# Kernel tuning notes

Hardware: AMD Instinct MI355X
Metric: run time of the kernel (lower is better)

The kernel has to match this reference:

```python
import jax, jax.numpy as jnp
import numpy as np

K_ORDER = 3
GRID_N = 10
GRID_LO, GRID_HI = -2.0, 2.0
LAYERS = [(49, 256), (256, 256), (256, 10)]
NCOEF = GRID_N + K_ORDER  # 13


def mish(x):
    return x * jnp.tanh(jax.nn.softplus(x))


def bspline_basis(x):
    # x: (B, in) -> basis (B, in, GRID_N + K_ORDER)
    h = (GRID_HI - GRID_LO) / GRID_N
    knots = GRID_LO + h * jnp.arange(-K_ORDER, GRID_N + K_ORDER + 1, dtype=x.dtype)  # (G+2k+1,)
    xx = x[..., None]
    B = ((xx >= knots[:-1]) & (xx < knots[1:])).astype(x.dtype)  # degree-0, (B,in,G+2k)
    for d in range(1, K_ORDER + 1):
        left = (xx - knots[: -(d + 1)]) / (knots[d:-1] - knots[: -(d + 1)]) * B[..., :-1]
        right = (knots[d + 1:] - xx) / (knots[d + 1:] - knots[1:-d]) * B[..., 1:]
        B = left + right
    return B  # (B, in, G+k)


def kan_layer(x, coef, scale_base, scale_sp, bias):
    # x: (B,in); coef: (in,out,G+k); scales: (in,out); bias: (out,)
    basis = bspline_basis(x)                                   # (B,in,G+k)
    spline = jnp.einsum('big,iog->bo', basis, coef * scale_sp[..., None])
    base = jnp.einsum('bi,io->bo', mish(x), scale_base)
    return base + spline + bias


def setup_inputs() -> dict:
    key = jax.random.key(0)
    ks = jax.random.split(key, 1 + 4 * len(LAYERS))
    inp = {'x': jax.random.normal(ks[0], (8192, 1, 28, 28), dtype=jnp.float32)}
    i = 1
    for li, (fin, fout) in enumerate(LAYERS, start=1):
        inp[f'coef{li}'] = 0.1 * jax.random.normal(ks[i], (fin, fout, NCOEF), dtype=jnp.float32); i += 1
        inp[f'sb{li}'] = 1.0 + 0.1 * jax.random.normal(ks[i], (fin, fout), dtype=jnp.float32); i += 1
        inp[f'sp{li}'] = 1.0 + 0.1 * jax.random.normal(ks[i], (fin, fout), dtype=jnp.float32); i += 1
        inp[f'b{li}'] = jnp.zeros((fout,), dtype=jnp.float32); i += 1
    return inp


def reference(x, coef1, sb1, sp1, b1, coef2, sb2, sp2, b2, coef3, sb3, sp3, b3):
    B = x.shape[0]
    # avg_pool2d(x, 4): 28x28 -> 7x7
    h = x.reshape(B, 1, 7, 4, 7, 4).mean(axis=(3, 5))
    h = h.reshape(B, 49)
    h = kan_layer(h, coef1, sb1, sp1, b1)
    h = kan_layer(h, coef2, sb2, sp2, b2)
    h = kan_layer(h, coef3, sb3, sp3, b3)
    return jax.nn.log_softmax(h, axis=1)
```

## Files before the change

kernel.cpp:

```cpp
#include <hip/hip_runtime.h>
#include <hip/hip_bf16.h>

typedef __bf16 bf16x8_t __attribute__((ext_vector_type(8)));
typedef float f32x4_t __attribute__((ext_vector_type(4)));
using bf16 = __hip_bfloat16;

__device__ __forceinline__ unsigned short f2bf_bits(float v) {
  __hip_bfloat16 h = __float2bfloat16(v);
  return *reinterpret_cast<unsigned short*>(&h);
}

__device__ __forceinline__ float mish_f(float x) {
  float z = __expf(x);
  float n = z * (z + 2.0f);
  float m = x * n / (n + 2.0f);
  return (x > 10.0f) ? x : m;
}

__device__ __forceinline__ void bar() {
  asm volatile("s_waitcnt lgkmcnt(0)" ::: "memory");
  __builtin_amdgcn_s_barrier();
  asm volatile("" ::: "memory");
}

__device__ __forceinline__ void kan_feats28(bf16* dst, float x) {
  float t = (x + 3.2f) * 2.5f;
  const bool inr = (t >= 0.0f) && (t < 16.0f);
  float tc = inr ? t : 0.0f;
  float tf = floorf(tc);
  const int j0 = (int)tf - 3;
  float u = tc - tf;
  float um = 1.0f - u;
  float u2 = u * u, u3 = u2 * u;
  const float s6 = 1.0f / 6.0f;
  float w0 = um * um * um * s6;
  float w1 = (3.0f * u3 - 6.0f * u2 + 4.0f) * s6;
  float w2 = (-3.0f * u3 + 3.0f * u2 + 3.0f * u + 1.0f) * s6;
  float w3 = u3 * s6;
  if (!inr) { w0 = 0.f; w1 = 0.f; w2 = 0.f; w3 = 0.f; }
  const unsigned int b0 = f2bf_bits(w0), b1 = f2bf_bits(w1);
  const unsigned int b2 = f2bf_bits(w2), b3 = f2bf_bits(w3);
  const unsigned int bm = f2bf_bits(mish_f(x));
  unsigned int* d32 = (unsigned int*)dst;
#pragma unroll
  for (int dd = 0; dd < 7; ++dd) {
    const int r = 2 * dd - j0;
    unsigned int lo = (r == 0) ? b0 : (r == 1) ? b1 : (r == 2) ? b2 : (r == 3) ? b3 : 0u;
    unsigned int hi;
    if (dd < 6) {
      const int r1 = r + 1;
      hi = (r1 == 0) ? b0 : (r1 == 1) ? b1 : (r1 == 2) ? b2 : (r1 == 3) ? b3 : 0u;
    } else {
      hi = bm;
    }
    d32[dd] = lo | (hi << 16);
  }
}

__global__ __launch_bounds__(256) void prep_all(
    const float* __restrict__ c1, const float* __restrict__ sb1, const float* __restrict__ sp1,
    const float* __restrict__ c2, const float* __restrict__ sb2, const float* __restrict__ sp2,
    const float* __restrict__ c3, const float* __restrict__ sb3, const float* __restrict__ sp3,
    bf16* __restrict__ W1f, bf16* __restrict__ W2f, bf16* __restrict__ W3f) {
  const int b = blockIdx.x, t = threadIdx.x;
  float vals[14];
  if (b < 49) {
    const int i = b, o = t;
    const int ntg = o >> 4, lrr = o & 15;
    const size_t io = (size_t)i * 256 + o;
    const float spv = sp1[io];
#pragma unroll
    for (int r = 0; r < 13; ++r) vals[r] = c1[io * 13 + r] * spv;
    vals[13] = sb1[io];
#pragma unroll
    for (int d = 0; d < 7; ++d) {
      const int k2 = i * 14 + 2 * d;
      const int s = k2 >> 5, r2 = k2 & 31;
      const size_t off = ((size_t)(s * 16 + ntg)) * 512 + lrr * 32 + (r2 >> 3) * 8 + (r2 & 7);
      *(unsigned int*)(W1f + off) = (unsigned int)f2bf_bits(vals[2 * d]) |
                                    ((unsigned int)f2bf_bits(vals[2 * d + 1]) << 16);
    }
  } else if (b == 49) {
    const int ntg = t >> 4, lrr = t & 15;
#pragma unroll
    for (int d = 0; d < 9; ++d) {
      const int k2 = 686 + 2 * d;
      const int r2 = k2 & 31;
      *(unsigned int*)(W1f + ((size_t)(21 * 16 + ntg)) * 512 + lrr * 32 + (r2 >> 3) * 8 + (r2 & 7)) = 0u;
    }
  } else if (b < 306) {
    const int i = b - 50;
    const int o = t;
    const int ntg = o >> 4, lrr = o & 15;
    const size_t io = (size_t)i * 256 + o;
    const float spv = sp2[io];
#pragma unroll
    for (int r = 0; r < 13; ++r) vals[r] = c2[io * 13 + r] * spv;
    vals[13] = sb2[io];
#pragma unroll
    for (int d = 0; d < 7; ++d) {
      const int k2 = i * 14 + 2 * d;
      const int s = k2 >> 5, r2 = k2 & 31;
      const size_t off = ((size_t)(s * 16 + ntg)) * 512 + lrr * 32 + (r2 >> 3) * 8 + (r2 & 7);
      *(unsigned int*)(W2f + off) = (unsigned int)f2bf_bits(vals[2 * d]) |
                                    ((unsigned int)f2bf_bits(vals[2 * d + 1]) << 16);
    }
  } else {
    const int idx = (b - 306) * 256 + t;
    const int i = idx >> 4, o = idx & 15;
    if (o < 10) {
      const size_t io = (size_t)i * 10 + o;
      const float spv = sp3[io];
#pragma unroll
      for (int r = 0; r < 13; ++r) vals[r] = c3[io * 13 + r] * spv;
      vals[13] = sb3[io];
#pragma unroll
      for (int d = 0; d < 7; ++d) {
        const int k2 = i * 14 + 2 * d;
        const int s = k2 >> 5, r2 = k2 & 31;
        const size_t off = (size_t)s * 512 + o * 32 + (r2 >> 3) * 8 + (r2 & 7);
        *(unsigned int*)(W3f + off) = (unsigned int)f2bf_bits(vals[2 * d]) |
                                      ((unsigned int)f2bf_bits(vals[2 * d + 1]) << 16);
      }
    } else {
#pragma unroll
      for (int d = 0; d < 7; ++d) {
        const int k2 = i * 14 + 2 * d;
        const int s = k2 >> 5, r2 = k2 & 31;
        *(unsigned int*)(W3f + (size_t)s * 512 + o * 32 + (r2 >> 3) * 8 + (r2 & 7)) = 0u;
      }
    }
  }
}

__global__ __launch_bounds__(1024, 4) void meganet(
    const float* __restrict__ x, const bf16* __restrict__ W1f,
    const bf16* __restrict__ W2f, const bf16* __restrict__ W3f,
    const float* __restrict__ b1, const float* __restrict__ b2,
    const float* __restrict__ b3, float* __restrict__ out) {
  __shared__ __align__(16) char lds[73728];
  float* const Hs = (float*)lds;
  bf16* const Ach0 = (bf16*)(lds + 36864);
  bf16* const Ach1 = (bf16*)(lds + 51712);
  float* const P = (float*)(lds + 66560);
  float* const xs = (float*)lds;
  float* const Red = (float*)(lds + 36864);
  float* const V = (float*)(lds + 51712);

  const int t = threadIdx.x;
  const int w = t >> 6, lane = t & 63, quad = lane >> 4, lr = lane & 15;
  const int tr = (t >> 4) & 31, ej = t & 15;
  const int r0 = blockIdx.x * 32;
  const int foff = lr * 32 + quad * 8;
  const bool cons = (w < 8);
  const int ntg0 = 2 * w;

  for (int h = 0; h < 2; ++h) {
    const float4* src = (const float4*)x + (size_t)(r0 + h * 16) * 196;
    float4* xd = (float4*)xs;
#pragma unroll
    for (int l = 0; l < 4; ++l) {
      const int idx = t + l * 1024;
      if (idx < 3136) xd[idx] = src[idx];
    }
    bar();
    if (t < 784) {
      const int img = t / 49, p = t - img * 49;
      const int oh = p / 7, ow = p - oh * 7;
      const float* xi = xs + img * 784 + oh * 112 + ow * 4;
      f32x4_t s4 = (f32x4_t){0.f, 0.f, 0.f, 0.f};
#pragma unroll
      for (int rr = 0; rr < 4; ++rr) {
        const f32x4_t v = *(const f32x4_t*)(xi + rr * 28);
        s4 += v;
      }
      P[(h * 16 + img) * 56 + p] = (s4[0] + s4[1] + s4[2] + s4[3]) * (1.0f / 16.0f);
    }
    bar();
  }

  f32x4_t acc[2][2];
#pragma unroll
  for (int m = 0; m < 2; ++m)
#pragma unroll
    for (int n = 0; n < 2; ++n) acc[m][n] = (f32x4_t){0.f, 0.f, 0.f, 0.f};

  bf16x8_t q0[4], q1[4];
  if (cons) {
#pragma unroll
    for (int s = 0; s < 4; ++s) {
      q0[s] = *(const bf16x8_t*)(W1f + (size_t)(s * 16 + ntg0) * 512 + foff);
      q1[s] = *(const bf16x8_t*)(W1f + (size_t)(s * 16 + ntg0 + 1) * 512 + foff);
    }
  } else {
    kan_feats28(Ach0 + tr * 232 + ej * 14, P[tr * 56 + ej]);
  }
  bar();
#pragma unroll
  for (int c = 0; c < 4; ++c) {
    const bf16* const Ac = (c & 1) ? Ach1 : Ach0;
    bf16* const An = (c & 1) ? Ach0 : Ach1;
    if (cons) {
      const int nks = (c < 3) ? 7 : 1;
#pragma unroll
      for (int ks = 0; ks < 7; ++ks) {
        if (ks >= nks) continue;
        const int kk = c * 7 + ks;
        const int sl = kk & 3;
        bf16x8_t bb0 = q0[sl], bb1 = q1[sl];
        if (kk + 4 < 22) {
          q0[sl] = *(const bf16x8_t*)(W1f + (size_t)((kk + 4) * 16 + ntg0) * 512 + foff);
          q1[sl] = *(const bf16x8_t*)(W1f + (size_t)((kk + 4) * 16 + ntg0 + 1) * 512 + foff);
        }
#pragma unroll
        for (int m = 0; m < 2; ++m) {
          bf16x8_t a = *(const bf16x8_t*)(Ac + (m * 16 + lr) * 232 + ks * 32 + quad * 8);
          acc[m][0] = __builtin_amdgcn_mfma_f32_16x16x32_bf16(a, bb0, acc[m][0], 0, 0, 0);
          acc[m][1] = __builtin_amdgcn_mfma_f32_16x16x32_bf16(a, bb1, acc[m][1], 0, 0, 0);
        }
      }
    } else {
      if (c < 2) {
        kan_feats28(An + tr * 232 + ej * 14, P[tr * 56 + (c + 1) * 16 + ej]);
      } else if (c == 2) {
        if (ej == 0) kan_feats28(An + tr * 232, P[tr * 56 + 48]);
        else if (ej == 1) {
          unsigned int* z = (unsigned int*)(An + tr * 232 + 14);
#pragma unroll
          for (int d = 0; d < 9; ++d) z[d] = 0u;
        }
      }
    }
    bar();
  }
  if (cons) {
#pragma unroll
    for (int m = 0; m < 2; ++m)
#pragma unroll
      for (int n = 0; n < 2; ++n) {
        const int col = w * 32 + n * 16 + lr;
        const float bn = b1[col];
        f32x4_t v;
#pragma unroll
        for (int r = 0; r < 4; ++r) v[r] = acc[m][n][r] + bn;
        *(f32x4_t*)(Hs + col * 36 + m * 16 + quad * 4) = v;
      }
  }
  bar();

#pragma unroll
  for (int m = 0; m < 2; ++m)
#pragma unroll
    for (int n = 0; n < 2; ++n) acc[m][n] = (f32x4_t){0.f, 0.f, 0.f, 0.f};
  if (cons) {
#pragma unroll
    for (int s = 0; s < 4; ++s) {
      q0[s] = *(const bf16x8_t*)(W2f + (size_t)(s * 16 + ntg0) * 512 + foff);
      q1[s] = *(const bf16x8_t*)(W2f + (size_t)(s * 16 + ntg0 + 1) * 512 + foff);
    }
  } else {
    kan_feats28(Ach0 + tr * 232 + ej * 14, Hs[ej * 36 + tr]);
  }
  bar();
#pragma unroll
  for (int c = 0; c < 16; ++c) {
    const bf16* const Ac = (c & 1) ? Ach1 : Ach0;
    bf16* const An = (c & 1) ? Ach0 : Ach1;
    if (cons) {
#pragma unroll
      for (int ks = 0; ks < 7; ++ks) {
        const int kk = c * 7 + ks;
        const int sl = kk & 3;
        bf16x8_t bb0 = q0[sl], bb1 = q1[sl];
        if (kk + 4 < 112) {
          q0[sl] = *(const bf16x8_t*)(W2f + (size_t)((kk + 4) * 16 + ntg0) * 512 + foff);
          q1[sl] = *(const bf16x8_t*)(W2f + (size_t)((kk + 4) * 16 + ntg0 + 1) * 512 + foff);
        }
#pragma unroll
        for (int m = 0; m < 2; ++m) {
          bf16x8_t a = *(const bf16x8_t*)(Ac + (m * 16 + lr) * 232 + ks * 32 + quad * 8);
          acc[m][0] = __builtin_amdgcn_mfma_f32_16x16x32_bf16(a, bb0, acc[m][0], 0, 0, 0);
          acc[m][1] = __builtin_amdgcn_mfma_f32_16x16x32_bf16(a, bb1, acc[m][1], 0, 0, 0);
        }
      }
    } else if (c < 15) {
      kan_feats28(An + tr * 232 + ej * 14, Hs[((c + 1) * 16 + ej) * 36 + tr]);
    }
    bar();
  }
  if (cons) {
#pragma unroll
    for (int m = 0; m < 2; ++m)
#pragma unroll
      for (int n = 0; n < 2; ++n) {
        const int col = w * 32 + n * 16 + lr;
        const float bn = b2[col];
        f32x4_t v;
#pragma unroll
        for (int r = 0; r < 4; ++r) v[r] = acc[m][n][r] + bn;
        *(f32x4_t*)(Hs + col * 36 + m * 16 + quad * 4) = v;
      }
  }
  bar();

  f32x4_t acc3[2];
  acc3[0] = (f32x4_t){0.f, 0.f, 0.f, 0.f};
  acc3[1] = acc3[0];
  bf16x8_t q3[4];
  if (w < 7) {
#pragma unroll
    for (int s = 0; s < 4; ++s)
      q3[s] = *(const bf16x8_t*)(W3f + (size_t)(s * 7 + w) * 512 + foff);
  } else if (!cons) {
    kan_feats28(Ach0 + tr * 232 + ej * 14, Hs[ej * 36 + tr]);
  }
  bar();
#pragma unroll
  for (int c = 0; c < 16; ++c) {
    const bf16* const Ac = (c & 1) ? Ach1 : Ach0;
    bf16* const An = (c & 1) ? Ach0 : Ach1;
    if (w < 7) {
      bf16x8_t bb = q3[c & 3];
      if (c + 4 < 16)
        q3[c & 3] = *(const bf16x8_t*)(W3f + (size_t)((c + 4) * 7 + w) * 512 + foff);
#pragma unroll
      for (int m = 0; m < 2; ++m) {
        bf16x8_t a = *(const bf16x8_t*)(Ac + (m * 16 + lr) * 232 + w * 32 + quad * 8);
        acc3[m] = __builtin_amdgcn_mfma_f32_16x16x32_bf16(a, bb, acc3[m], 0, 0, 0);
      }
    } else if (!cons && c < 15) {
      kan_feats28(An + tr * 232 + ej * 14, Hs[((c + 1) * 16 + ej) * 36 + tr]);
    }
    bar();
  }
  if (w < 7) {
#pragma unroll
    for (int m = 0; m < 2; ++m)
#pragma unroll
      for (int r = 0; r < 4; ++r)
        Red[w * 512 + (m * 16 + quad * 4 + r) * 16 + lr] = acc3[m][r];
  }
  bar();
  if (t < 512) {
    float s = (ej < 10) ? b3[ej] : 0.f;
#pragma unroll
    for (int ks = 0; ks < 7; ++ks) s += Red[ks * 512 + tr * 16 + ej];
    V[tr * 16 + ej] = s;
  }
  bar();
  if (t < 32) {
    float vv[10];
#pragma unroll
    for (int o = 0; o < 10; ++o) vv[o] = V[t * 16 + o];
    float mx = vv[0];
#pragma unroll
    for (int o = 1; o < 10; ++o) mx = fmaxf(mx, vv[o]);
    float se = 0.f;
#pragma unroll
    for (int o = 0; o < 10; ++o) se += expf(vv[o] - mx);
    const float l = mx + logf(se);
#pragma unroll
    for (int o = 0; o < 10; ++o) out[(size_t)(r0 + t) * 10 + o] = vv[o] - l;
  }
}

extern "C" void kernel_launch(void* const* d_in, const int* in_sizes, int n_in,
                              void* d_out, int out_size, void* d_ws, size_t ws_size,
                              hipStream_t stream) {
  const float* x = (const float*)d_in[0];
  const float* coef1 = (const float*)d_in[1];
  const float* sb1 = (const float*)d_in[2];
  const float* sp1 = (const float*)d_in[3];
  const float* b1 = (const float*)d_in[4];
  const float* coef2 = (const float*)d_in[5];
  const float* sb2 = (const float*)d_in[6];
  const float* sp2 = (const float*)d_in[7];
  const float* b2 = (const float*)d_in[8];
  const float* coef3 = (const float*)d_in[9];
  const float* sb3 = (const float*)d_in[10];
  const float* sp3 = (const float*)d_in[11];
  const float* b3 = (const float*)d_in[12];
  float* out = (float*)d_out;

  char* ws = (char*)d_ws;
  bf16* W1f = (bf16*)ws;
  bf16* W2f = (bf16*)(ws + 360448);
  bf16* W3f = (bf16*)(ws + 2195456);

  prep_all<<<322, 256, 0, stream>>>(coef1, sb1, sp1, coef2, sb2, sp2,
                                    coef3, sb3, sp3, W1f, W2f, W3f);
  meganet<<<256, 1024, 0, stream>>>(x, W1f, W2f, W3f, b1, b2, b3, out);
}
```

Before: 154.6 us.

## Deepen weight prefetch ring and pin global loads with sched barriers

The register prefetch ring for layer-1 and layer-2 weight fragments grows from 4 to 6 stages. Each K-step is rewritten as a macro that issues the next global load before the LDS reads and MFMAs, with a sched_barrier that keeps the compiler from sinking the VMEM loads. The B-spline feature writer is also simplified to zero the row and then store up to four weights directly, instead of running a select chain per dword. The deeper ring raises VGPR pressure, and the branchy scattered 16-bit LDS stores could cost more than the old packed 32-bit writes.

```diff
diff --git a/kernel.cpp b/kernel.cpp
--- a/kernel.cpp
+++ b/kernel.cpp
@@ -23,38 +23,67 @@
   asm volatile("" ::: "memory");
 }
 
+#define SB_PIN_VMEM() __builtin_amdgcn_sched_barrier(0x38F)
+
+#define KSTEP2(WPTR, AC, KK, KS, NKK)                                          \
+  do {                                                                         \
+    bf16x8_t nb0_, nb1_;                                                       \
+    if ((NKK) >= 0) {                                                          \
+      const bf16* p_ = (WPTR) + (size_t)((NKK) * 16 + ntg0) * 512 + foff;      \
+      nb0_ = *(const bf16x8_t*)p_;                                             \
+      nb1_ = *(const bf16x8_t*)(p_ + 512);                                     \
+    }                                                                          \
+    SB_PIN_VMEM();                                                             \
+    bf16x8_t a0_ = *(const bf16x8_t*)((AC) + lr * 232 + (KS) * 32 + quad * 8); \
+    bf16x8_t a1_ =                                                             \
+        *(const bf16x8_t*)((AC) + (16 + lr) * 232 + (KS) * 32 + quad * 8);     \
+    bf16x8_t b0_ = q0[(KK) % 6];                                               \
+    bf16x8_t b1_ = q1[(KK) % 6];                                               \
+    acc[0][0] = __builtin_amdgcn_mfma_f32_16x16x32_bf16(a0_, b0_, acc[0][0], 0, 0, 0); \
+    acc[0][1] = __builtin_amdgcn_mfma_f32_16x16x32_bf16(a0_, b1_, acc[0][1], 0, 0, 0); \
+    acc[1][0] = __builtin_amdgcn_mfma_f32_16x16x32_bf16(a1_, b0_, acc[1][0], 0, 0, 0); \
+    acc[1][1] = __builtin_amdgcn_mfma_f32_16x16x32_bf16(a1_, b1_, acc[1][1], 0, 0, 0); \
+    if ((NKK) >= 0) { q0[(KK) % 6] = nb0_; q1[(KK) % 6] = nb1_; }              \
+  } while (0)
+
+#define KSTEP1(AC, CC, NKK)                                                    \
+  do {                                                                         \
+    bf16x8_t nb_;                                                              \
+    if ((NKK) >= 0) {                                                          \
+      nb_ = *(const bf16x8_t*)(W3f + (size_t)((NKK) * 7 + w) * 512 + foff);    \
+    }                                                                          \
+    SB_PIN_VMEM();                                                             \
+    bf16x8_t a0_ = *(const bf16x8_t*)((AC) + lr * 232 + w * 32 + quad * 8);    \
+    bf16x8_t a1_ = *(const bf16x8_t*)((AC) + (16 + lr) * 232 + w * 32 + quad * 8); \
+    bf16x8_t b_ = q3[(CC) % 4];                                                \
+    acc3[0] = __builtin_amdgcn_mfma_f32_16x16x32_bf16(a0_, b_, acc3[0], 0, 0, 0); \
+    acc3[1] = __builtin_amdgcn_mfma_f32_16x16x32_bf16(a1_, b_, acc3[1], 0, 0, 0); \
+    if ((NKK) >= 0) q3[(CC) % 4] = nb_;                                        \
+  } while (0)
+
 __device__ __forceinline__ void kan_feats28(bf16* dst, float x) {
+  unsigned int* d32 = (unsigned int*)dst;
+#pragma unroll
+  for (int d = 0; d < 7; ++d) d32[d] = 0u;
   float t = (x + 3.2f) * 2.5f;
-  const bool inr = (t >= 0.0f) && (t < 16.0f);
-  float tc = inr ? t : 0.0f;
-  float tf = floorf(tc);
-  const int j0 = (int)tf - 3;
-  float u = tc - tf;
-  float um = 1.0f - u;
-  float u2 = u * u, u3 = u2 * u;
-  const float s6 = 1.0f / 6.0f;
-  float w0 = um * um * um * s6;
-  float w1 = (3.0f * u3 - 6.0f * u2 + 4.0f) * s6;
-  float w2 = (-3.0f * u3 + 3.0f * u2 + 3.0f * u + 1.0f) * s6;
-  float w3 = u3 * s6;
-  if (!inr) { w0 = 0.f; w1 = 0.f; w2 = 0.f; w3 = 0.f; }
-  const unsigned int b0 = f2bf_bits(w0), b1 = f2bf_bits(w1);
-  const unsigned int b2 = f2bf_bits(w2), b3 = f2bf_bits(w3);
-  const unsigned int bm = f2bf_bits(mish_f(x));
-  unsigned int* d32 = (unsigned int*)dst;
-#pragma unroll
-  for (int dd = 0; dd < 7; ++dd) {
-    const int r = 2 * dd - j0;
-    unsigned int lo = (r == 0) ? b0 : (r == 1) ? b1 : (r == 2) ? b2 : (r == 3) ? b3 : 0u;
-    unsigned int hi;
-    if (dd < 6) {
-      const int r1 = r + 1;
-      hi = (r1 == 0) ? b0 : (r1 == 1) ? b1 : (r1 == 2) ? b2 : (r1 == 3) ? b3 : 0u;
-    } else {
-      hi = bm;
-    }
-    d32[dd] = lo | (hi << 16);
-  }
+  if (t >= 0.0f && t < 16.0f) {
+    float tf = floorf(t);
+    int c = (int)tf;
+    float u = t - tf;
+    float um = 1.0f - u;
+    float u2 = u * u, u3 = u2 * u;
+    const float s6 = 1.0f / 6.0f;
+    float w0 = um * um * um * s6;
+    float w1 = (3.0f * u3 - 6.0f * u2 + 4.0f) * s6;
+    float w2 = (-3.0f * u3 + 3.0f * u2 + 3.0f * u + 1.0f) * s6;
+    float w3 = u3 * s6;
+    int j0 = c - 3;
+    if (j0 >= 0)               dst[j0]     = __float2bfloat16(w0);
+    if (j0 >= -1 && j0 <= 11)  dst[j0 + 1] = __float2bfloat16(w1);
+    if (j0 >= -2 && j0 <= 10)  dst[j0 + 2] = __float2bfloat16(w2);
+    if (j0 <= 9)               dst[j0 + 3] = __float2bfloat16(w3);
+  }
+  dst[13] = __float2bfloat16(mish_f(x));
 }
 
 __global__ __launch_bounds__(256) void prep_all(
@@ -185,13 +214,16 @@
 #pragma unroll
     for (int n = 0; n < 2; ++n) acc[m][n] = (f32x4_t){0.f, 0.f, 0.f, 0.f};
 
-  bf16x8_t q0[4], q1[4];
+  bf16x8_t q0[6], q1[6];
+
   if (cons) {
 #pragma unroll
-    for (int s = 0; s < 4; ++s) {
-      q0[s] = *(const bf16x8_t*)(W1f + (size_t)(s * 16 + ntg0) * 512 + foff);
-      q1[s] = *(const bf16x8_t*)(W1f + (size_t)(s * 16 + ntg0 + 1) * 512 + foff);
-    }
+    for (int s = 0; s < 6; ++s) {
+      const bf16* p_ = W1f + (size_t)(s * 16 + ntg0) * 512 + foff;
+      q0[s] = *(const bf16x8_t*)p_;
+      q1[s] = *(const bf16x8_t*)(p_ + 512);
+    }
+    SB_PIN_VMEM();
   } else {
     kan_feats28(Ach0 + tr * 232 + ej * 14, P[tr * 56 + ej]);
   }
@@ -201,23 +233,22 @@
     const bf16* const Ac = (c & 1) ? Ach1 : Ach0;
     bf16* const An = (c & 1) ? Ach0 : Ach1;
     if (cons) {
-      const int nks = (c < 3) ? 7 : 1;
-#pragma unroll
-      for (int ks = 0; ks < 7; ++ks) {
-        if (ks >= nks) continue;
-        const int kk = c * 7 + ks;
-        const int sl = kk & 3;
-        bf16x8_t bb0 = q0[sl], bb1 = q1[sl];
-        if (kk + 4 < 22) {
-          q0[sl] = *(const bf16x8_t*)(W1f + (size_t)((kk + 4) * 16 + ntg0) * 512 + foff);
-          q1[sl] = *(const bf16x8_t*)(W1f + (size_t)((kk + 4) * 16 + ntg0 + 1) * 512 + foff);
+      if (c < 2) {
+#pragma unroll
+        for (int ks = 0; ks < 7; ++ks) {
+          const int kk = c * 7 + ks;
+          KSTEP2(W1f, Ac, kk, ks, kk + 6);
         }
-#pragma unroll
-        for (int m = 0; m < 2; ++m) {
-          bf16x8_t a = *(const bf16x8_t*)(Ac + (m * 16 + lr) * 232 + ks * 32 + quad * 8);
-          acc[m][0] = __builtin_amdgcn_mfma_f32_16x16x32_bf16(a, bb0, acc[m][0], 0, 0, 0);
-          acc[m][1] = __builtin_amdgcn_mfma_f32_16x16x32_bf16(a, bb1, acc[m][1], 0, 0, 0);
-        }
+      } else if (c == 2) {
+        KSTEP2(W1f, Ac, 14, 0, 20);
+        KSTEP2(W1f, Ac, 15, 1, 21);
+        KSTEP2(W1f, Ac, 16, 2, -1);
+        KSTEP2(W1f, Ac, 17, 3, -1);
+        KSTEP2(W1f, Ac, 18, 4, -1);
+        KSTEP2(W1f, Ac, 19, 5, -1);
+        KSTEP2(W1f, Ac, 20, 6, -1);
+      } else {
+        KSTEP2(W1f, Ac, 21, 0, -1);
       }
     } else {
       if (c < 2) {
@@ -254,10 +285,12 @@
     for (int n = 0; n < 2; ++n) acc[m][n] = (f32x4_t){0.f, 0.f, 0.f, 0.f};
   if (cons) {
 #pragma unroll
-    for (int s = 0; s < 4; ++s) {
-      q0[s] = *(const bf16x8_t*)(W2f + (size_t)(s * 16 + ntg0) * 512 + foff);
-      q1[s] = *(const bf16x8_t*)(W2f + (size_t)(s * 16 + ntg0 + 1) * 512 + foff);
-    }
+    for (int s = 0; s < 6; ++s) {
+      const bf16* p_ = W2f + (size_t)(s * 16 + ntg0) * 512 + foff;
+      q0[s] = *(const bf16x8_t*)p_;
+      q1[s] = *(const bf16x8_t*)(p_ + 512);
+    }
+    SB_PIN_VMEM();
   } else {
     kan_feats28(Ach0 + tr * 232 + ej * 14, Hs[ej * 36 + tr]);
   }
@@ -267,21 +300,20 @@
     const bf16* const Ac = (c & 1) ? Ach1 : Ach0;
     bf16* const An = (c & 1) ? Ach0 : Ach1;
     if (cons) {
-#pragma unroll
-      for (int ks = 0; ks < 7; ++ks) {
-        const int kk = c * 7 + ks;
-        const int sl = kk & 3;
-        bf16x8_t bb0 = q0[sl], bb1 = q1[sl];
-        if (kk + 4 < 112) {
-          q0[sl] = *(const bf16x8_t*)(W2f + (size_t)((kk + 4) * 16 + ntg0) * 512 + foff);
-          q1[sl] = *(const bf16x8_t*)(W2f + (size_t)((kk + 4) * 16 + ntg0 + 1) * 512 + foff);
+      if (c < 15) {
+#pragma unroll
+        for (int ks = 0; ks < 7; ++ks) {
+          const int kk = c * 7 + ks;
+          KSTEP2(W2f, Ac, kk, ks, kk + 6);
         }
-#pragma unroll
-        for (int m = 0; m < 2; ++m) {
-          bf16x8_t a = *(const bf16x8_t*)(Ac + (m * 16 + lr) * 232 + ks * 32 + quad * 8);
-          acc[m][0] = __builtin_amdgcn_mfma_f32_16x16x32_bf16(a, bb0, acc[m][0], 0, 0, 0);
-          acc[m][1] = __builtin_amdgcn_mfma_f32_16x16x32_bf16(a, bb1, acc[m][1], 0, 0, 0);
-        }
+      } else {
+        KSTEP2(W2f, Ac, 105, 0, 111);
+        KSTEP2(W2f, Ac, 106, 1, -1);
+        KSTEP2(W2f, Ac, 107, 2, -1);
+        KSTEP2(W2f, Ac, 108, 3, -1);
+        KSTEP2(W2f, Ac, 109, 4, -1);
+        KSTEP2(W2f, Ac, 110, 5, -1);
+        KSTEP2(W2f, Ac, 111, 6, -1);
       }
     } else if (c < 15) {
       kan_feats28(An + tr * 232 + ej * 14, Hs[((c + 1) * 16 + ej) * 36 + tr]);
@@ -311,6 +343,7 @@
 #pragma unroll
     for (int s = 0; s < 4; ++s)
       q3[s] = *(const bf16x8_t*)(W3f + (size_t)(s * 7 + w) * 512 + foff);
+    SB_PIN_VMEM();
   } else if (!cons) {
     kan_feats28(Ach0 + tr * 232 + ej * 14, Hs[ej * 36 + tr]);
   }
@@ -320,14 +353,8 @@
     const bf16* const Ac = (c & 1) ? Ach1 : Ach0;
     bf16* const An = (c & 1) ? Ach0 : Ach1;
     if (w < 7) {
-      bf16x8_t bb = q3[c & 3];
-      if (c + 4 < 16)
-        q3[c & 3] = *(const bf16x8_t*)(W3f + (size_t)((c + 4) * 7 + w) * 512 + foff);
-#pragma unroll
-      for (int m = 0; m < 2; ++m) {
-        bf16x8_t a = *(const bf16x8_t*)(Ac + (m * 16 + lr) * 232 + w * 32 + quad * 8);
-        acc3[m] = __builtin_amdgcn_mfma_f32_16x16x32_bf16(a, bb, acc3[m], 0, 0, 0);
-      }
+      if (c <= 11) KSTEP1(Ac, c, c + 4);
+      else         KSTEP1(Ac, c, -1);
     } else if (!cons && c < 15) {
       kan_feats28(An + tr * 232 + ej * 14, Hs[((c + 1) * 16 + ej) * 36 + tr]);
     }
```

Result: slower. 169.2 us (+9.5%).
